# Optimization experiments

Hardware: AMD Instinct MI355X
Metric: run time of the kernel (lower is better)

## Reference

```python
import jax, jax.numpy as jnp
import numpy as np

B, TX, TY, D, H = 8, 128, 128, 512, 512
LN_EPS = 1e-3  # keras LayerNormalization default epsilon


def setup_inputs() -> dict:
    key = jax.random.key(0)
    ks = jax.random.split(key, 6)
    scale = 1.0 / np.sqrt(D)
    return {
        "context": jax.random.normal(ks[0], (B, TX, D), jnp.float32),
        "x": jax.random.normal(ks[1], (B, TY, D), jnp.float32),
        "Wa": jax.random.normal(ks[2], (D, H), jnp.float32) * scale,
        "bWa": jnp.zeros((H,), jnp.float32),
        "Ua": jax.random.normal(ks[3], (D, H), jnp.float32) * scale,
        "bUa": jnp.zeros((H,), jnp.float32),
        "Va": jax.random.normal(ks[4], (H, 1), jnp.float32) * (1.0 / np.sqrt(H)),
        "bVa": jnp.zeros((1,), jnp.float32),
        "gamma": jnp.ones((D,), jnp.float32),
        "beta": jnp.zeros((D,), jnp.float32),
    }


def reference(context, x, Wa, bWa, Ua, bUa, Va, bVa, gamma, beta):
    # context: [B,Tx,D], x: [B,Ty,D]
    Wc = context @ Wa + bWa                      # [B,Tx,H]
    Ux = x @ Ua + bUa                            # [B,Ty,H]
    t = jnp.tanh(Wc[:, None, :, :] + Ux[:, :, None, :])  # [B,Ty,Tx,H]
    scores = jnp.einsum('btxh,h->btx', t, Va[:, 0]) + bVa[0]  # [B,Ty,Tx]
    attn = jax.nn.softmax(scores, axis=-1)
    cv = jnp.einsum('btx,bxd->btd', attn, context)  # [B,Ty,D]
    mean = jnp.mean(cv, axis=-1, keepdims=True)
    var = jnp.mean(jnp.square(cv - mean), axis=-1, keepdims=True)
    cv = (cv - mean) * jax.lax.rsqrt(var + LN_EPS) * gamma + beta
    return cv + x
```

## Files before the change

### kernel.cpp

```cpp
#include <hip/hip_runtime.h>


#define SCALE 2.8853900817779268f

typedef __attribute__((ext_vector_type(8))) short short8;
typedef float floatx4 __attribute__((ext_vector_type(4)));

__device__ __forceinline__ unsigned pack_bf_trunc(float lo, float hi) {
  return __builtin_amdgcn_perm(__float_as_uint(hi), __float_as_uint(lo),
                               0x07060302u);
}

__device__ __forceinline__ unsigned pack_bf_rne(float lo, float hi) {
  unsigned ul = __float_as_uint(lo), uh = __float_as_uint(hi);
  ul += 0x7fffu + ((ul >> 16) & 1u);
  uh += 0x7fffu + ((uh >> 16) & 1u);
  return __builtin_amdgcn_perm(uh, ul, 0x07060302u);
}

__global__ __launch_bounds__(512) void gemm_all(
    const float* __restrict__ ctx, const float* __restrict__ xin,
    const float* __restrict__ Wa, const float* __restrict__ Ua,
    const float* __restrict__ bWa, const float* __restrict__ bUa,
    unsigned* __restrict__ WcT, float* __restrict__ Ux) {
  const bool second = (blockIdx.z != 0);
  const float* __restrict__ A = second ? xin : ctx;
  const float* __restrict__ W = second ? Ua : Wa;
  const int m0 = blockIdx.x * 32, n0 = blockIdx.y * 64;

  __shared__ __align__(16) unsigned short As[512 * 8];
  __shared__ __align__(16) unsigned short Bs[1024 * 8];

  const int t = threadIdx.x;
  const int lane = t & 63, wv = t >> 6;

  const int arow = ((t >> 6) & 1) * 16 + (t & 15);
  const int ak   = (t >> 7) * 32 + ((t & 63) >> 4) * 8;
  const float* aptr = A + (size_t)(m0 + arow) * 512 + ak;

  const int bn0_ = ((t >> 6) & 3) * 16 + (t & 15);
  const int bk0_ = (t >> 8) * 32 + ((t & 63) >> 4) * 8;
  const int s2 = t + 512;
  const int bn1_ = ((s2 >> 6) & 3) * 16 + (s2 & 15);
  const int bk1_ = (s2 >> 8) * 32 + ((s2 & 63) >> 4) * 8;
  const float* bptr0 = W + (size_t)bk0_ * 512 + n0 + bn0_;
  const float* bptr1 = W + (size_t)bk1_ * 512 + n0 + bn1_;

  const int wm = wv & 1, wn = wv >> 1;
  floatx4 acc = {};

  float4 a0 = *(const float4*)(aptr);
  float4 a1 = *(const float4*)(aptr + 4);
  float bw0[8], bw1[8];
#pragma unroll
  for (int j = 0; j < 8; j++) {
    bw0[j] = bptr0[(size_t)j * 512];
    bw1[j] = bptr1[(size_t)j * 512];
  }

  for (int kt = 0; kt < 512; kt += 128) {
    union { short8 s; uint4 u; } av, bv0, bv1;
    av.u.x = pack_bf_trunc(a0.x, a0.y);
    av.u.y = pack_bf_trunc(a0.z, a0.w);
    av.u.z = pack_bf_trunc(a1.x, a1.y);
    av.u.w = pack_bf_trunc(a1.z, a1.w);
    bv0.u.x = pack_bf_trunc(bw0[0], bw0[1]);
    bv0.u.y = pack_bf_trunc(bw0[2], bw0[3]);
    bv0.u.z = pack_bf_trunc(bw0[4], bw0[5]);
    bv0.u.w = pack_bf_trunc(bw0[6], bw0[7]);
    bv1.u.x = pack_bf_trunc(bw1[0], bw1[1]);
    bv1.u.y = pack_bf_trunc(bw1[2], bw1[3]);
    bv1.u.z = pack_bf_trunc(bw1[4], bw1[5]);
    bv1.u.w = pack_bf_trunc(bw1[6], bw1[7]);
    ((short8*)As)[t] = av.s;
    ((short8*)Bs)[t] = bv0.s;
    ((short8*)Bs)[t + 512] = bv1.s;
    __syncthreads();
    if (kt + 128 < 512) {
      a0 = *(const float4*)(aptr + kt + 128);
      a1 = *(const float4*)(aptr + kt + 132);
      const float* p0 = bptr0 + (size_t)(kt + 128) * 512;
      const float* p1 = bptr1 + (size_t)(kt + 128) * 512;
#pragma unroll
      for (int j = 0; j < 8; j++) {
        bw0[j] = p0[(size_t)j * 512];
        bw1[j] = p1[(size_t)j * 512];
      }
    }
#pragma unroll
    for (int ks = 0; ks < 4; ks++) {
      const short8 af = ((const short8*)As)[ks * 128 + wm * 64 + lane];
      const short8 bf = ((const short8*)Bs)[ks * 256 + wn * 64 + lane];
      acc = __builtin_amdgcn_mfma_f32_16x16x32_bf16(af, bf, acc, 0, 0, 0);
    }
    __syncthreads();
  }

  const int quad = lane >> 4;
  const int h = n0 + wn * 16 + (lane & 15);
  const int mg0 = m0 + wm * 16 + quad * 4;
  if (!second) {
    const float bias = bWa[h] + bUa[h];
    const int b = mg0 >> 7, tx0 = mg0 & 127;
    unsigned pk[4];
#pragma unroll
    for (int r = 0; r < 4; r++) {
      const float v = (acc[r] + bias) * SCALE;
      const float vn = __shfl_xor(v, 1);
      pk[r] = pack_bf_rne(v, vn);
    }
    if ((lane & 1) == 0) {
      uint4 o; o.x = pk[0]; o.y = pk[1]; o.z = pk[2]; o.w = pk[3];
      *(uint4*)&WcT[(size_t)b * 32768 + (size_t)(h >> 1) * 128 + tx0] = o;
    }
  } else {
#pragma unroll
    for (int r = 0; r < 4; r++)
      Ux[(size_t)(mg0 + r) * 512 + h] = acc[r] * SCALE;
  }
}

__global__ __launch_bounds__(1024) void attn4(
    const unsigned* __restrict__ WcT, const float* __restrict__ Ux,
    const float* __restrict__ ctx, const float* __restrict__ xin,
    const float* __restrict__ Va,
    const float* __restrict__ gamma, const float* __restrict__ beta,
    float* __restrict__ out) {
  const int b = blockIdx.x >> 5;
  const int ty0 = (blockIdx.x & 31) * 4;
  const int t = threadIdx.x;
  const int lane = t & 63, wv = t >> 6;

  __shared__ __align__(16) float4 s_ux[512];
  __shared__ float s_va[512];
  __shared__ float s_part[32][128];
  __shared__ __align__(16) float4 s_at[128];
  __shared__ float s_red[4][2][8];
  __shared__ float s_mv[4][2];

  {
    const float* uxb = Ux + (size_t)(b * 128 + ty0) * 512;
    for (int i = t; i < 2048; i += 1024) {
      const int r = i >> 9, h = i & 511;
      ((float*)&s_ux[h])[r] = uxb[i];
    }
    if (t < 512) s_va[t] = Va[t];
  }
  __syncthreads();

  const int tx = t & 127, hq = t >> 7;
  {
    const unsigned* wp = WcT + (size_t)b * 32768 + (size_t)hq * 4096 + tx;
    float a0 = 0.f, a1 = 0.f, a2 = 0.f, a3 = 0.f;
#pragma unroll 4
    for (int hh = 0; hh < 32; hh++) {
      const unsigned u = wp[(size_t)hh * 128];
      const float w0 = __uint_as_float(u << 16);
      const float w1 = __uint_as_float(u & 0xffff0000u);
      const int h = hq * 64 + hh * 2;
      const float4 u0 = s_ux[h];
      const float4 u1 = s_ux[h + 1];
      const float va0 = s_va[h], va1 = s_va[h + 1];
      a0 = fmaf(va0, __builtin_amdgcn_rcpf(1.0f + __builtin_amdgcn_exp2f(w0 + u0.x)), a0);
      a1 = fmaf(va0, __builtin_amdgcn_rcpf(1.0f + __builtin_amdgcn_exp2f(w0 + u0.y)), a1);
      a2 = fmaf(va0, __builtin_amdgcn_rcpf(1.0f + __builtin_amdgcn_exp2f(w0 + u0.z)), a2);
      a3 = fmaf(va0, __builtin_amdgcn_rcpf(1.0f + __builtin_amdgcn_exp2f(w0 + u0.w)), a3);
      a0 = fmaf(va1, __builtin_amdgcn_rcpf(1.0f + __builtin_amdgcn_exp2f(w1 + u1.x)), a0);
      a1 = fmaf(va1, __builtin_amdgcn_rcpf(1.0f + __builtin_amdgcn_exp2f(w1 + u1.y)), a1);
      a2 = fmaf(va1, __builtin_amdgcn_rcpf(1.0f + __builtin_amdgcn_exp2f(w1 + u1.z)), a2);
      a3 = fmaf(va1, __builtin_amdgcn_rcpf(1.0f + __builtin_amdgcn_exp2f(w1 + u1.w)), a3);
    }
    s_part[hq * 4 + 0][tx] = a0;
    s_part[hq * 4 + 1][tx] = a1;
    s_part[hq * 4 + 2][tx] = a2;
    s_part[hq * 4 + 3][tx] = a3;
  }
  __syncthreads();

  if (wv < 4) {
    const int r = wv;
    float sA = 0.f, sB = 0.f;
#pragma unroll
    for (int q = 0; q < 8; q++) {
      sA += s_part[q * 4 + r][lane];
      sB += s_part[q * 4 + r][lane + 64];
    }
    sA *= -2.0f; sB *= -2.0f;
    float m = fmaxf(sA, sB);
#pragma unroll
    for (int off = 32; off; off >>= 1) m = fmaxf(m, __shfl_xor(m, off));
    const float eA = __expf(sA - m);
    const float eB = __expf(sB - m);
    float sm = eA + eB;
#pragma unroll
    for (int off = 32; off; off >>= 1) sm += __shfl_xor(sm, off);
    const float inv = __builtin_amdgcn_rcpf(sm);
    ((float*)&s_at[lane])[r] = eA * inv;
    ((float*)&s_at[lane + 64])[r] = eB * inv;
  }
  __syncthreads();

  const int d = t & 511, rh = t >> 9;
  float cv0 = 0.f, cv1 = 0.f;
  {
    const float* cp = ctx + (size_t)b * 65536 + d;
#pragma unroll 4
    for (int x = 0; x < 128; x++) {
      const float c = cp[(size_t)x * 512];
      const float2 at = *(const float2*)((const float*)&s_at[x] + rh * 2);
      cv0 = fmaf(at.x, c, cv0);
      cv1 = fmaf(at.y, c, cv1);
    }
  }

  const int wh = wv & 7;
#pragma unroll
  for (int j = 0; j < 2; j++) {
    const float v = j ? cv1 : cv0;
    float sm = v, q = v * v;
#pragma unroll
    for (int off = 32; off; off >>= 1) {
      sm += __shfl_xor(sm, off);
      q += __shfl_xor(q, off);
    }
    if (lane == 0) {
      s_red[rh * 2 + j][0][wh] = sm;
      s_red[rh * 2 + j][1][wh] = q;
    }
  }
  __syncthreads();
  if (t < 4) {
    float sm = 0.f, q = 0.f;
#pragma unroll
    for (int i = 0; i < 8; i++) { sm += s_red[t][0][i]; q += s_red[t][1][i]; }
    const float mean = sm * (1.0f / 512.0f);
    const float var = q * (1.0f / 512.0f) - mean * mean;
    s_mv[t][0] = mean;
    s_mv[t][1] = __builtin_amdgcn_rsqf(var + 1e-3f);
  }
  __syncthreads();

  {
    const float g = gamma[d], bb = beta[d];
#pragma unroll
    for (int j = 0; j < 2; j++) {
      const int r = rh * 2 + j;
      const int row = b * 128 + ty0 + r;
      const float v = j ? cv1 : cv0;
      const float xv = xin[(size_t)row * 512 + d];
      out[(size_t)row * 512 + d] = (v - s_mv[r][0]) * s_mv[r][1] * g + bb + xv;
    }
  }
}

extern "C" void kernel_launch(void* const* d_in, const int* in_sizes, int n_in,
                              void* d_out, int out_size, void* d_ws, size_t ws_size,
                              hipStream_t stream) {
  const float* ctx   = (const float*)d_in[0];
  const float* xin   = (const float*)d_in[1];
  const float* Wa    = (const float*)d_in[2];
  const float* bWa   = (const float*)d_in[3];
  const float* Ua    = (const float*)d_in[4];
  const float* bUa   = (const float*)d_in[5];
  const float* Va    = (const float*)d_in[6];
  const float* gamma = (const float*)d_in[8];
  const float* beta  = (const float*)d_in[9];
  float* out = (float*)d_out;

  char* ws = (char*)d_ws;
  unsigned* WcT = (unsigned*)ws;
  float* Ux = (float*)(ws + (1u << 20));

  gemm_all<<<dim3(32, 8, 2), 512, 0, stream>>>(ctx, xin, Wa, Ua, bWa, bUa, WcT, Ux);
  attn4<<<256, 1024, 0, stream>>>(WcT, Ux, ctx, xin, Va, gamma, beta, out);
}
```

Measured before the change: 108.7 us.

## Fuse projection GEMM and attention kernels into one cooperative launch with grid sync

Measured after the change: 243.0 us. 124% more time.

```diff
diff --git a/kernel.cpp b/kernel.cpp
--- a/kernel.cpp
+++ b/kernel.cpp
@@ -1,4 +1,5 @@
 #include <hip/hip_runtime.h>
+#include <hip/hip_cooperative_groups.h>
 
 
 #define SCALE 2.8853900817779268f
@@ -18,125 +19,130 @@
   return __builtin_amdgcn_perm(uh, ul, 0x07060302u);
 }
 
-__global__ __launch_bounds__(512) void gemm_all(
+__global__ __launch_bounds__(1024) void fused_all(
     const float* __restrict__ ctx, const float* __restrict__ xin,
-    const float* __restrict__ Wa, const float* __restrict__ Ua,
-    const float* __restrict__ bWa, const float* __restrict__ bUa,
-    unsigned* __restrict__ WcT, float* __restrict__ Ux) {
-  const bool second = (blockIdx.z != 0);
-  const float* __restrict__ A = second ? xin : ctx;
-  const float* __restrict__ W = second ? Ua : Wa;
-  const int m0 = blockIdx.x * 32, n0 = blockIdx.y * 64;
-
-  __shared__ __align__(16) unsigned short As[512 * 8];
-  __shared__ __align__(16) unsigned short Bs[1024 * 8];
-
-  const int t = threadIdx.x;
-  const int lane = t & 63, wv = t >> 6;
-
-  const int arow = ((t >> 6) & 1) * 16 + (t & 15);
-  const int ak   = (t >> 7) * 32 + ((t & 63) >> 4) * 8;
-  const float* aptr = A + (size_t)(m0 + arow) * 512 + ak;
-
-  const int bn0_ = ((t >> 6) & 3) * 16 + (t & 15);
-  const int bk0_ = (t >> 8) * 32 + ((t & 63) >> 4) * 8;
-  const int s2 = t + 512;
-  const int bn1_ = ((s2 >> 6) & 3) * 16 + (s2 & 15);
-  const int bk1_ = (s2 >> 8) * 32 + ((s2 & 63) >> 4) * 8;
-  const float* bptr0 = W + (size_t)bk0_ * 512 + n0 + bn0_;
-  const float* bptr1 = W + (size_t)bk1_ * 512 + n0 + bn1_;
-
-  const int wm = wv & 1, wn = wv >> 1;
-  floatx4 acc = {};
-
-  float4 a0 = *(const float4*)(aptr);
-  float4 a1 = *(const float4*)(aptr + 4);
-  float bw0[8], bw1[8];
-#pragma unroll
-  for (int j = 0; j < 8; j++) {
-    bw0[j] = bptr0[(size_t)j * 512];
-    bw1[j] = bptr1[(size_t)j * 512];
-  }
-
-  for (int kt = 0; kt < 512; kt += 128) {
-    union { short8 s; uint4 u; } av, bv0, bv1;
-    av.u.x = pack_bf_trunc(a0.x, a0.y);
-    av.u.y = pack_bf_trunc(a0.z, a0.w);
-    av.u.z = pack_bf_trunc(a1.x, a1.y);
-    av.u.w = pack_bf_trunc(a1.z, a1.w);
-    bv0.u.x = pack_bf_trunc(bw0[0], bw0[1]);
-    bv0.u.y = pack_bf_trunc(bw0[2], bw0[3]);
-    bv0.u.z = pack_bf_trunc(bw0[4], bw0[5]);
-    bv0.u.w = pack_bf_trunc(bw0[6], bw0[7]);
-    bv1.u.x = pack_bf_trunc(bw1[0], bw1[1]);
-    bv1.u.y = pack_bf_trunc(bw1[2], bw1[3]);
-    bv1.u.z = pack_bf_trunc(bw1[4], bw1[5]);
-    bv1.u.w = pack_bf_trunc(bw1[6], bw1[7]);
-    ((short8*)As)[t] = av.s;
-    ((short8*)Bs)[t] = bv0.s;
-    ((short8*)Bs)[t + 512] = bv1.s;
-    __syncthreads();
-    if (kt + 128 < 512) {
-      a0 = *(const float4*)(aptr + kt + 128);
-      a1 = *(const float4*)(aptr + kt + 132);
-      const float* p0 = bptr0 + (size_t)(kt + 128) * 512;
-      const float* p1 = bptr1 + (size_t)(kt + 128) * 512;
-#pragma unroll
-      for (int j = 0; j < 8; j++) {
-        bw0[j] = p0[(size_t)j * 512];
-        bw1[j] = p1[(size_t)j * 512];
-      }
-    }
-#pragma unroll
-    for (int ks = 0; ks < 4; ks++) {
-      const short8 af = ((const short8*)As)[ks * 128 + wm * 64 + lane];
-      const short8 bf = ((const short8*)Bs)[ks * 256 + wn * 64 + lane];
-      acc = __builtin_amdgcn_mfma_f32_16x16x32_bf16(af, bf, acc, 0, 0, 0);
-    }
-    __syncthreads();
-  }
-
-  const int quad = lane >> 4;
-  const int h = n0 + wn * 16 + (lane & 15);
-  const int mg0 = m0 + wm * 16 + quad * 4;
-  if (!second) {
-    const float bias = bWa[h] + bUa[h];
-    const int b = mg0 >> 7, tx0 = mg0 & 127;
-    unsigned pk[4];
-#pragma unroll
-    for (int r = 0; r < 4; r++) {
-      const float v = (acc[r] + bias) * SCALE;
-      const float vn = __shfl_xor(v, 1);
-      pk[r] = pack_bf_rne(v, vn);
-    }
-    if ((lane & 1) == 0) {
-      uint4 o; o.x = pk[0]; o.y = pk[1]; o.z = pk[2]; o.w = pk[3];
-      *(uint4*)&WcT[(size_t)b * 32768 + (size_t)(h >> 1) * 128 + tx0] = o;
-    }
-  } else {
-#pragma unroll
-    for (int r = 0; r < 4; r++)
-      Ux[(size_t)(mg0 + r) * 512 + h] = acc[r] * SCALE;
-  }
-}
-
-__global__ __launch_bounds__(1024) void attn4(
-    const unsigned* __restrict__ WcT, const float* __restrict__ Ux,
-    const float* __restrict__ ctx, const float* __restrict__ xin,
+    const float* __restrict__ Wa, const float* __restrict__ bWa,
+    const float* __restrict__ Ua, const float* __restrict__ bUa,
     const float* __restrict__ Va,
     const float* __restrict__ gamma, const float* __restrict__ beta,
+    unsigned* __restrict__ WcT, float* __restrict__ Ux,
     float* __restrict__ out) {
-  const int b = blockIdx.x >> 5;
-  const int ty0 = (blockIdx.x & 31) * 4;
   const int t = threadIdx.x;
-  const int lane = t & 63, wv = t >> 6;
-
+  const int lane = t & 63;
+
+  __shared__ __align__(16) unsigned short As2[2][512 * 8];
+  __shared__ __align__(16) unsigned short Bs2[2][1024 * 8];
   __shared__ __align__(16) float4 s_ux[512];
   __shared__ float s_va[512];
   __shared__ float s_part[32][128];
   __shared__ __align__(16) float4 s_at[128];
   __shared__ float s_red[4][2][8];
   __shared__ float s_mv[4][2];
+
+  {
+    const int half = t >> 9, tl = t & 511;
+    const int lb = (blockIdx.x << 1) | half;
+    const bool second = (lb >> 8) != 0;
+    const float* __restrict__ A = second ? xin : ctx;
+    const float* __restrict__ W = second ? Ua : Wa;
+    const int m0 = (lb & 31) * 32, n0 = ((lb >> 5) & 7) * 64;
+
+    unsigned short* As = As2[half];
+    unsigned short* Bs = Bs2[half];
+
+    const int arow = ((tl >> 6) & 1) * 16 + (tl & 15);
+    const int ak   = (tl >> 7) * 32 + ((tl & 63) >> 4) * 8;
+    const float* aptr = A + (size_t)(m0 + arow) * 512 + ak;
+
+    const int bn0_ = ((tl >> 6) & 3) * 16 + (tl & 15);
+    const int bk0_ = (tl >> 8) * 32 + ((tl & 63) >> 4) * 8;
+    const int s2 = tl + 512;
+    const int bn1_ = ((s2 >> 6) & 3) * 16 + (s2 & 15);
+    const int bk1_ = (s2 >> 8) * 32 + ((s2 & 63) >> 4) * 8;
+    const float* bptr0 = W + (size_t)bk0_ * 512 + n0 + bn0_;
+    const float* bptr1 = W + (size_t)bk1_ * 512 + n0 + bn1_;
+
+    const int wvl = tl >> 6;
+    const int wm = wvl & 1, wn = wvl >> 1;
+    floatx4 acc = {};
+
+    float4 a0 = *(const float4*)(aptr);
+    float4 a1 = *(const float4*)(aptr + 4);
+    float bw0[8], bw1[8];
+#pragma unroll
+    for (int j = 0; j < 8; j++) {
+      bw0[j] = bptr0[(size_t)j * 512];
+      bw1[j] = bptr1[(size_t)j * 512];
+    }
+
+    for (int kt = 0; kt < 512; kt += 128) {
+      union { short8 s; uint4 u; } av, bv0, bv1;
+      av.u.x = pack_bf_trunc(a0.x, a0.y);
+      av.u.y = pack_bf_trunc(a0.z, a0.w);
+      av.u.z = pack_bf_trunc(a1.x, a1.y);
+      av.u.w = pack_bf_trunc(a1.z, a1.w);
+      bv0.u.x = pack_bf_trunc(bw0[0], bw0[1]);
+      bv0.u.y = pack_bf_trunc(bw0[2], bw0[3]);
+      bv0.u.z = pack_bf_trunc(bw0[4], bw0[5]);
+      bv0.u.w = pack_bf_trunc(bw0[6], bw0[7]);
+      bv1.u.x = pack_bf_trunc(bw1[0], bw1[1]);
+      bv1.u.y = pack_bf_trunc(bw1[2], bw1[3]);
+      bv1.u.z = pack_bf_trunc(bw1[4], bw1[5]);
+      bv1.u.w = pack_bf_trunc(bw1[6], bw1[7]);
+      ((short8*)As)[tl] = av.s;
+      ((short8*)Bs)[tl] = bv0.s;
+      ((short8*)Bs)[tl + 512] = bv1.s;
+      __syncthreads();
+      if (kt + 128 < 512) {
+        a0 = *(const float4*)(aptr + kt + 128);
+        a1 = *(const float4*)(aptr + kt + 132);
+        const float* p0 = bptr0 + (size_t)(kt + 128) * 512;
+        const float* p1 = bptr1 + (size_t)(kt + 128) * 512;
+#pragma unroll
+        for (int j = 0; j < 8; j++) {
+          bw0[j] = p0[(size_t)j * 512];
+          bw1[j] = p1[(size_t)j * 512];
+        }
+      }
+#pragma unroll
+      for (int ks = 0; ks < 4; ks++) {
+        const short8 af = ((const short8*)As)[ks * 128 + wm * 64 + lane];
+        const short8 bf = ((const short8*)Bs)[ks * 256 + wn * 64 + lane];
+        acc = __builtin_amdgcn_mfma_f32_16x16x32_bf16(af, bf, acc, 0, 0, 0);
+      }
+      __syncthreads();
+    }
+
+    const int quad = lane >> 4;
+    const int h = n0 + wn * 16 + (lane & 15);
+    const int mg0 = m0 + wm * 16 + quad * 4;
+    if (!second) {
+      const float bias = bWa[h] + bUa[h];
+      const int b = mg0 >> 7, tx0 = mg0 & 127;
+      unsigned pk[4];
+#pragma unroll
+      for (int r = 0; r < 4; r++) {
+        const float v = (acc[r] + bias) * SCALE;
+        const float vn = __shfl_xor(v, 1);
+        pk[r] = pack_bf_rne(v, vn);
+      }
+      if ((lane & 1) == 0) {
+        uint4 o; o.x = pk[0]; o.y = pk[1]; o.z = pk[2]; o.w = pk[3];
+        *(uint4*)&WcT[(size_t)b * 32768 + (size_t)(h >> 1) * 128 + tx0] = o;
+      }
+    } else {
+#pragma unroll
+      for (int r = 0; r < 4; r++)
+        Ux[(size_t)(mg0 + r) * 512 + h] = acc[r] * SCALE;
+    }
+  }
+
+  __threadfence();
+  cooperative_groups::this_grid().sync();
+
+  const int b = blockIdx.x >> 5;
+  const int ty0 = (blockIdx.x & 31) * 4;
+  const int wv = t >> 6;
 
   {
     const float* uxb = Ux + (size_t)(b * 128 + ty0) * 512;
@@ -271,6 +277,8 @@
   unsigned* WcT = (unsigned*)ws;
   float* Ux = (float*)(ws + (1u << 20));
 
-  gemm_all<<<dim3(32, 8, 2), 512, 0, stream>>>(ctx, xin, Wa, Ua, bWa, bUa, WcT, Ux);
-  attn4<<<256, 1024, 0, stream>>>(WcT, Ux, ctx, xin, Va, gamma, beta, out);
-}
+  void* args[] = {&ctx, &xin, &Wa, &bWa, &Ua, &bUa, &Va, &gamma, &beta,
+                  &WcT, &Ux, &out};
+  hipLaunchCooperativeKernel((const void*)fused_all, dim3(256), dim3(1024),
+                             args, 0, stream);
+}
```
